# Optimization experiments

Hardware: AMD Instinct MI355X
Metric: run time of the kernel (lower is better)

## Reference

```python
import jax, jax.numpy as jnp
import numpy as np

B, S, H = 2, 1024, 2048
F_DIM = 1408        # per-expert ffn dim
SF_DIM = 5632       # shared expert ffn dim
E = 8               # num_experts
TOP_K = 2
NORM_TOPK_PROB = False


def setup_inputs() -> dict:
    key = jax.random.key(0)
    ks = jax.random.split(key, 9)
    w = lambda k, shp: (jax.random.normal(k, shp, dtype=jnp.float32) * 0.02)
    return {
        "hidden_states": jax.random.normal(ks[0], (B, S, H), dtype=jnp.float32),
        "gate_w": w(ks[1], (E, H)),                 # router Linear(H -> E), no bias
        "gate_proj_w": w(ks[2], (E, F_DIM, H)),     # stacked expert gate_proj weights
        "up_proj_w": w(ks[3], (E, F_DIM, H)),
        "down_proj_w": w(ks[4], (E, H, F_DIM)),
        "shared_gate_proj_w": w(ks[5], (SF_DIM, H)),
        "shared_up_proj_w": w(ks[6], (SF_DIM, H)),
        "shared_down_proj_w": w(ks[7], (H, SF_DIM)),
        "shared_expert_gate_w": w(ks[8], (1, H)),   # Linear(H -> 1), no bias
    }


def reference(hidden_states, gate_w, gate_proj_w, up_proj_w, down_proj_w,
              shared_gate_proj_w, shared_up_proj_w, shared_down_proj_w,
              shared_expert_gate_w):
    b, s, h = hidden_states.shape
    x = hidden_states.reshape(-1, h)                              # [T, H]
    # router: softmax in fp32 -> top_k
    logits = x @ gate_w.T                                         # [T, E]
    probs = jax.nn.softmax(logits.astype(jnp.float32), axis=-1)
    rw, sel = jax.lax.top_k(probs, TOP_K)                         # [T, K]
    if NORM_TOPK_PROB:
        rw = rw / jnp.sum(rw, axis=-1, keepdims=True)
    rw = rw.astype(x.dtype)
    # dense one-hot dispatch weights [T, E]
    wm = jnp.sum(jax.nn.one_hot(sel, E, dtype=rw.dtype) * rw[..., None], axis=1)
    # all experts on all tokens (dense dispatch, as in the original)
    g = jax.nn.silu(jnp.einsum('th,efh->tef', x, gate_proj_w))    # [T, E, F]
    u = jnp.einsum('th,efh->tef', x, up_proj_w)
    routed = jnp.einsum('tef,ehf,te->th', g * u, down_proj_w, wm) # [T, H]
    # shared expert with scalar sigmoid gate
    sg = jax.nn.silu(x @ shared_gate_proj_w.T) * (x @ shared_up_proj_w.T)
    shared = sg @ shared_down_proj_w.T                            # [T, H]
    gate_val = jax.nn.sigmoid(x @ shared_expert_gate_w.T)         # [T, 1]
    out = routed + gate_val * shared
    return out.reshape(b, s, h)
```

## Files before the change

kernel.cpp:

```cpp
#include <hip/hip_runtime.h>

#define TT 2048
#define HD 2048
#define FD 1408
#define SFD 5632
#define NE 8
#define BM 128
#define BN 128
#define BK 32

using f32x4 = __attribute__((ext_vector_type(4))) float;
using s16x8 = __attribute__((ext_vector_type(8))) short;
typedef unsigned short us;

__device__ __forceinline__ us f2bf(float f) {
    union { float f; unsigned u; } v; v.f = f;
    unsigned r = v.u + 0x7fff + ((v.u >> 16) & 1);
    return (us)(r >> 16);
}
__device__ __forceinline__ float bf2f(us u) {
    union { unsigned u; float f; } v; v.u = ((unsigned)u) << 16;
    return v.f;
}
__device__ __forceinline__ unsigned cvt2(float a, float b) {
    union { float f; unsigned u; } va, vb; va.f = a; vb.f = b;
    unsigned ra = va.u + 0x8000u, rb = vb.u + 0x8000u;
    return (rb & 0xffff0000u) | (ra >> 16);
}
__device__ __forceinline__ s16x8 pack8(f32x4 h0, f32x4 h1) {
    union { unsigned u[4]; s16x8 s; } r;
    r.u[0] = cvt2(h0[0], h0[1]); r.u[1] = cvt2(h0[2], h0[3]);
    r.u[2] = cvt2(h1[0], h1[1]); r.u[3] = cvt2(h1[2], h1[3]);
    return r.s;
}

__device__ __forceinline__ void gload16(const void* g, void* l) {
    __builtin_amdgcn_global_load_lds(
        (const __attribute__((address_space(1))) unsigned*)g,
        (__attribute__((address_space(3))) unsigned*)l, 16, 0, 0);
}

__global__ void cvt_kernel(const float* __restrict__ x, us* __restrict__ xb) {
    size_t i = ((size_t)blockIdx.x * 256 + threadIdx.x) * 8;
    float4 f0 = *(const float4*)(x + i);
    float4 f1 = *(const float4*)(x + i + 4);
    s16x8 v;
    v[0]=(short)f2bf(f0.x); v[1]=(short)f2bf(f0.y); v[2]=(short)f2bf(f0.z); v[3]=(short)f2bf(f0.w);
    v[4]=(short)f2bf(f1.x); v[5]=(short)f2bf(f1.y); v[6]=(short)f2bf(f1.z); v[7]=(short)f2bf(f1.w);
    *(s16x8*)(xb + i) = v;
}

__global__ void router_kernel(const float* __restrict__ x, const float* __restrict__ gw,
                              const float* __restrict__ segw,
                              int* counts, int* tlist, float* wlist, float* gateval,
                              int* selpos) {
    int wave = threadIdx.x >> 6;
    int lane = threadIdx.x & 63;
    int t = blockIdx.x * 4 + wave;
    float acc[9];
    #pragma unroll
    for (int i = 0; i < 9; ++i) acc[i] = 0.f;
    const float* xrow = x + (size_t)t * HD;
    for (int h = lane; h < HD; h += 64) {
        float xv = xrow[h];
        #pragma unroll
        for (int e = 0; e < NE; ++e) acc[e] += xv * gw[e * HD + h];
        acc[8] += xv * segw[h];
    }
    #pragma unroll
    for (int i = 0; i < 9; ++i) {
        float v = acc[i];
        #pragma unroll
        for (int s = 32; s > 0; s >>= 1) v += __shfl_xor(v, s);
        acc[i] = v;
    }
    if (lane == 0) {
        float m = acc[0];
        #pragma unroll
        for (int e = 1; e < NE; ++e) m = fmaxf(m, acc[e]);
        float p[NE], sum = 0.f;
        #pragma unroll
        for (int e = 0; e < NE; ++e) { p[e] = expf(acc[e] - m); sum += p[e]; }
        float inv = 1.f / sum;
        int b1 = 0, b2 = -1; float v1 = p[0], v2 = -1.f;
        #pragma unroll
        for (int e = 1; e < NE; ++e) {
            if (p[e] > v1) { v2 = v1; b2 = b1; v1 = p[e]; b1 = e; }
            else if (p[e] > v2) { v2 = p[e]; b2 = e; }
        }
        v1 *= inv; v2 *= inv;
        int s1 = atomicAdd(&counts[b1], 1); tlist[b1 * TT + s1] = t; wlist[b1 * TT + s1] = v1;
        int s2 = atomicAdd(&counts[b2], 1); tlist[b2 * TT + s2] = t; wlist[b2 * TT + s2] = v2;
        selpos[2 * t]     = b1 * TT + s1;
        selpos[2 * t + 1] = b2 * TT + s2;
        gateval[t] = 1.f / (1.f + expf(-acc[8]));
    }
}

__global__ void prefix_kernel(const int* counts, int* offsets) {
    if (threadIdx.x == 0) {
        int s = 0;
        for (int e = 0; e < NE; ++e) { offsets[e] = s; s += counts[e]; }
    }
}

__global__ void combine_full(const int* __restrict__ selpos, const float* __restrict__ wlist,
                             const int* __restrict__ offsets, const float* __restrict__ gateval,
                             const float* __restrict__ sdpart, const us* __restrict__ robuf,
                             float* __restrict__ out) {
    int t = blockIdx.x;
    int p0 = selpos[2 * t], p1 = selpos[2 * t + 1];
    float w0 = wlist[p0], w1 = wlist[p1];
    int r0 = offsets[p0 >> 11] + (p0 & (TT - 1));
    int r1 = offsets[p1 >> 11] + (p1 & (TT - 1));
    float g = gateval[t];
    int c = threadIdx.x * 8;
    const float* s0 = sdpart + (size_t)t * HD + c;
    const float* s1 = sdpart + (size_t)TT * HD + (size_t)t * HD + c;
    s16x8 a = *(const s16x8*)(robuf + (size_t)r0 * HD + c);
    s16x8 b = *(const s16x8*)(robuf + (size_t)r1 * HD + c);
    float* op = out + (size_t)t * HD + c;
    #pragma unroll
    for (int j = 0; j < 8; ++j)
        op[j] = g * (s0[j] + s1[j]) + w0 * bf2f((us)a[j]) + w1 * bf2f((us)b[j]);
}

__global__ void combine_add(const int* __restrict__ selpos, const float* __restrict__ wlist,
                            const int* __restrict__ offsets,
                            const us* __restrict__ robuf, float* __restrict__ out) {
    int t = blockIdx.x;
    int p0 = selpos[2 * t], p1 = selpos[2 * t + 1];
    float w0 = wlist[p0], w1 = wlist[p1];
    int r0 = offsets[p0 >> 11] + (p0 & (TT - 1));
    int r1 = offsets[p1 >> 11] + (p1 & (TT - 1));
    int c = threadIdx.x * 8;
    s16x8 a = *(const s16x8*)(robuf + (size_t)r0 * HD + c);
    s16x8 b = *(const s16x8*)(robuf + (size_t)r1 * HD + c);
    float* op = out + (size_t)t * HD + c;
    #pragma unroll
    for (int j = 0; j < 8; ++j)
        op[j] += w0 * bf2f((us)a[j]) + w1 * bf2f((us)b[j]);
}

#define GU_TOT   2112
#define GU_CHUNK (GU_TOT / 8)
#define DN_TOT   2560
#define DN_CHUNK (DN_TOT / 8)

__global__ __launch_bounds__(256, 3)
void gemm6(const us* __restrict__ xb,
           const us* __restrict__ Bg_s, const us* __restrict__ Bu_s,
           const us* __restrict__ Bg_r, const us* __restrict__ Bu_r,
           us* __restrict__ Cs, us* __restrict__ Cr,
           const int* __restrict__ counts, const int* __restrict__ offsets,
           const int* __restrict__ tlist) {
    __shared__ s16x8 Asl[2][512];
    __shared__ s16x8 B0l[2][512];
    __shared__ s16x8 B1l[2][512];

    int hw = blockIdx.x;
    int flat = (hw & 7) * GU_CHUNK + (hw >> 3);
    int pi = flat >> 4, mt = flat & 15;
    int grpIdx = pi / 3, pos = pi % 3;
    int z, nt;
    if (pos == 0) { z = 0; nt = grpIdx; }
    else { int ri = grpIdx * 2 + (pos - 1);
           z = 1 + ri / 11; nt = ri % 11; }

    bool sp = (z == 0);
    int e = z - 1;
    int M = sp ? TT : counts[e];
    int n0 = nt * BN;
    int m0 = mt * BM;
    if (M == 0 || m0 >= M) return;
    int row_off = sp ? 0 : offsets[e];
    const us* B0p = sp ? Bg_s : Bg_r + (size_t)e * FD * HD;
    const us* B1p = sp ? Bu_s : Bu_r + (size_t)e * FD * HD;

    int tid = threadIdx.x;
    int lane = tid & 63, w = tid >> 6;

    const us* aptr[2];
    const us* b0ptr[2];
    const us* b1ptr[2];
    #pragma unroll
    for (int j = 0; j < 2; ++j) {
        int r = 32 * w + 16 * j + (lane >> 2);
        int c = (lane & 3) ^ ((r >> 1) & 3);
        int ar = m0 + r; if (ar > M - 1) ar = M - 1;
        size_t arow = sp ? (size_t)ar : (size_t)tlist[e * TT + ar];
        aptr[j]  = xb + arow * HD + c * 8;
        b0ptr[j] = B0p + (size_t)(n0 + r) * HD + c * 8;
        b1ptr[j] = B1p + (size_t)(n0 + r) * HD + c * 8;
    }

    int wm = (w >> 1) * 64, wn = (w & 1) * 64;
    int grp = lane >> 4, l16 = lane & 15;

    f32x4 acc0[4][4], acc1[4][4];
    f32x4 zero = {0.f, 0.f, 0.f, 0.f};
    #pragma unroll
    for (int mi = 0; mi < 4; ++mi)
        #pragma unroll
        for (int ni = 0; ni < 4; ++ni) { acc0[mi][ni] = zero; acc1[mi][ni] = zero; }

    auto stage = [&](int buf, int k0) {
        #pragma unroll
        for (int j = 0; j < 2; ++j)
            gload16(aptr[j] + k0, (void*)&Asl[buf][(32 * w + 16 * j) * 4]);
        #pragma unroll
        for (int j = 0; j < 2; ++j)
            gload16(b0ptr[j] + k0, (void*)&B0l[buf][(32 * w + 16 * j) * 4]);
        #pragma unroll
        for (int j = 0; j < 2; ++j)
            gload16(b1ptr[j] + k0, (void*)&B1l[buf][(32 * w + 16 * j) * 4]);
    };

    stage(0, 0);
    int cur = 0;
    const int NT = HD / BK;
    for (int kt = 0; kt < NT; ++kt) {
        __syncthreads();
        if (kt + 1 < NT) stage(cur ^ 1, (kt + 1) * BK);
        s16x8 af[4];
        #pragma unroll
        for (int mi = 0; mi < 4; ++mi) {
            int rr = wm + mi * 16 + l16;
            af[mi] = Asl[cur][rr * 4 + (grp ^ ((rr >> 1) & 3))];
        }
        #pragma unroll
        for (int ni = 0; ni < 4; ++ni) {
            int rb = wn + ni * 16 + l16;
            int slot = rb * 4 + (grp ^ ((rb >> 1) & 3));
            s16x8 b0 = B0l[cur][slot];
            #pragma unroll
            for (int mi = 0; mi < 4; ++mi)
                acc0[mi][ni] = __builtin_amdgcn_mfma_f32_16x16x32_bf16(af[mi], b0, acc0[mi][ni], 0, 0, 0);
            s16x8 b1 = B1l[cur][slot];
            #pragma unroll
            for (int mi = 0; mi < 4; ++mi)
                acc1[mi][ni] = __builtin_amdgcn_mfma_f32_16x16x32_bf16(af[mi], b1, acc1[mi][ni], 0, 0, 0);
        }
        cur ^= 1;
    }

    #pragma unroll
    for (int mi = 0; mi < 4; ++mi) {
        #pragma unroll
        for (int r_ = 0; r_ < 4; ++r_) {
            int mrow = m0 + wm + mi * 16 + (lane >> 4) * 4 + r_;
            if (mrow >= M) continue;
            #pragma unroll
            for (int ni = 0; ni < 4; ++ni) {
                int col = n0 + wn + ni * 16 + l16;
                float g = acc0[mi][ni][r_], u = acc1[mi][ni][r_];
                float val = g * u / (1.f + __expf(-g));
                if (sp) Cs[(size_t)mrow * SFD + col] = f2bf(val);
                else    Cr[(size_t)(row_off + mrow) * FD + col] = f2bf(val);
            }
        }
    }
}

__global__ __launch_bounds__(256, 3)
void gemm_down(const us* __restrict__ Ashared, const us* __restrict__ Arouted,
               const us* __restrict__ Bshared, const us* __restrict__ Brouted,
               float* __restrict__ Cshared, us* __restrict__ Crouted,
               const int* __restrict__ counts, const int* __restrict__ offsets) {
    __shared__ s16x8 Asl[2][512];
    __shared__ s16x8 Bsl[2][512];

    int hw = blockIdx.x;
    int flat = (hw & 7) * DN_CHUNK + (hw >> 3);
    int pi = flat >> 4, mt = flat & 15;
    int grpIdx = pi / 5, pos = pi % 5;
    int z, nt;
    if (pos == 0) { z = grpIdx >> 4; nt = grpIdx & 15; }
    else { int ri = grpIdx * 4 + (pos - 1);
           z = 2 + (ri >> 4); nt = ri & 15; }

    bool sp = (z < 2);
    int e = z - 2;
    int M = sp ? TT : counts[e];
    int n0 = nt * BN;
    int m0 = mt * BM;
    if (M == 0 || m0 >= M) return;
    int row_off = sp ? 0 : offsets[e];
    int NT = sp ? (SFD / 2 / BK) : (FD / BK);
    int lda = sp ? SFD : FD;
    int kofs = sp ? z * (SFD / 2) : 0;
    const us* Abase = (sp ? Ashared : Arouted) + kofs;
    const us* Bbase = (sp ? Bshared : Brouted + (size_t)e * HD * FD) + kofs;

    int tid = threadIdx.x;
    int lane = tid & 63, w = tid >> 6;

    const us* aptr[2];
    const us* bptr[2];
    #pragma unroll
    for (int j = 0; j < 2; ++j) {
        int r = 32 * w + 16 * j + (lane >> 2);
        int c = (lane & 3) ^ ((r >> 1) & 3);
        int ar = m0 + r; if (ar > M - 1) ar = M - 1;
        size_t arow = sp ? (size_t)ar : (size_t)(row_off + ar);
        aptr[j] = Abase + arow * lda + c * 8;
        bptr[j] = Bbase + (size_t)(n0 + r) * lda + c * 8;
    }

    int wm = (w >> 1) * 64, wn = (w & 1) * 64;
    int grp = lane >> 4, l16 = lane & 15;

    f32x4 acc[4][4];
    f32x4 zero = {0.f, 0.f, 0.f, 0.f};
    #pragma unroll
    for (int mi = 0; mi < 4; ++mi)
        #pragma unroll
        for (int ni = 0; ni < 4; ++ni) acc[mi][ni] = zero;

    auto stage = [&](int buf, int k0) {
        #pragma unroll
        for (int j = 0; j < 2; ++j)
            gload16(aptr[j] + k0, (void*)&Asl[buf][(32 * w + 16 * j) * 4]);
        #pragma unroll
        for (int j = 0; j < 2; ++j)
            gload16(bptr[j] + k0, (void*)&Bsl[buf][(32 * w + 16 * j) * 4]);
    };

    stage(0, 0);
    int cur = 0;
    for (int kt = 0; kt < NT; ++kt) {
        __syncthreads();
        if (kt + 1 < NT) stage(cur ^ 1, (kt + 1) * BK);
        s16x8 af[4];
        #pragma unroll
        for (int mi = 0; mi < 4; ++mi) {
            int rr = wm + mi * 16 + l16;
            af[mi] = Asl[cur][rr * 4 + (grp ^ ((rr >> 1) & 3))];
        }
        #pragma unroll
        for (int ni = 0; ni < 4; ++ni) {
            int rb = wn + ni * 16 + l16;
            s16x8 bf = Bsl[cur][rb * 4 + (grp ^ ((rb >> 1) & 3))];
            #pragma unroll
            for (int mi = 0; mi < 4; ++mi)
                acc[mi][ni] = __builtin_amdgcn_mfma_f32_16x16x32_bf16(af[mi], bf, acc[mi][ni], 0, 0, 0);
        }
        cur ^= 1;
    }

    #pragma unroll
    for (int mi = 0; mi < 4; ++mi) {
        #pragma unroll
        for (int r_ = 0; r_ < 4; ++r_) {
            int mrow = m0 + wm + mi * 16 + (lane >> 4) * 4 + r_;
            if (mrow >= M) continue;
            #pragma unroll
            for (int ni = 0; ni < 4; ++ni) {
                int col = n0 + wn + ni * 16 + l16;
                float v = acc[mi][ni][r_];
                if (sp) Cshared[(size_t)z * TT * HD + (size_t)mrow * HD + col] = v;
                else    Crouted[(size_t)(row_off + mrow) * HD + col] = f2bf(v);
            }
        }
    }
}

template<int EPI, bool GATHER>
__global__ __launch_bounds__(256, 2)
void gemm4(const us* __restrict__ A, int lda,
           const float* __restrict__ B, size_t eStrideB, int ldb, int K,
           int Mfixed, const int* __restrict__ counts, const int* __restrict__ offsets,
           const int* __restrict__ tlist, const float* __restrict__ wlist,
           us* __restrict__ C, int ldc,
           const float* __restrict__ gateval, float* __restrict__ out, int ldout) {
    __shared__ s16x8 As[3][512];
    __shared__ f32x4 Bs[3][1024];

    int e = blockIdx.z;
    int M = counts ? counts[e] : Mfixed;
    int n0 = blockIdx.x * BN;
    int m0 = blockIdx.y * BM;
    if (M == 0 || m0 >= M) return;
    int row_off = offsets ? offsets[e] : 0;
    const float* Bp = B + (size_t)e * eStrideB;

    int tid = threadIdx.x;
    int lane = tid & 63, w = tid >> 6;

    const us* aptr[2];
    #pragma unroll
    for (int j = 0; j < 2; ++j) {
        int r = 32 * w + 16 * j + (lane >> 2);
        int c = (lane & 3) ^ (r & 3);
        int ar = m0 + r; if (ar > M - 1) ar = M - 1;
        size_t grow;
        if constexpr (GATHER) grow = (size_t)tlist[e * TT + ar];
        else                  grow = (size_t)(row_off + ar);
        aptr[j] = A + grow * (size_t)lda + c * 8;
    }
    const float* bptr[4];
    #pragma unroll
    for (int j = 0; j < 4; ++j) {
        int r = 32 * w + 8 * j + (lane >> 3);
        int c = (lane & 7) ^ (r & 7);
        bptr[j] = Bp + (size_t)(n0 + r) * ldb + c * 4;
    }

    int wm = (w >> 1) * 64, wn = (w & 1) * 64;
    int grp = lane >> 4, l16 = lane & 15;

    f32x4 acc[4][4];
    f32x4 zero = {0.f, 0.f, 0.f, 0.f};
    #pragma unroll
    for (int mi = 0; mi < 4; ++mi)
        #pragma unroll
        for (int ni = 0; ni < 4; ++ni) acc[mi][ni] = zero;

    auto stage = [&](int buf, int k0) {
        #pragma unroll
        for (int j = 0; j < 2; ++j)
            gload16(aptr[j] + k0, (void*)&As[buf][(32 * w + 16 * j) * 4]);
        #pragma unroll
        for (int j = 0; j < 4; ++j)
            gload16(bptr[j] + k0, (void*)&Bs[buf][(32 * w + 8 * j) * 8]);
    };

    int NT = K / BK;
    stage(0, 0);
    stage(1, BK);
    for (int kt = 0; kt < NT; ++kt) {
        int cur = kt % 3;
        __builtin_amdgcn_s_barrier();
        if (kt + 2 < NT) {
            stage((kt + 2) % 3, (kt + 2) * BK);
            asm volatile("s_waitcnt vmcnt(12)" ::: "memory");
        } else if (kt + 1 < NT) {
            asm volatile("s_waitcnt vmcnt(6)" ::: "memory");
        } else {
            asm volatile("s_waitcnt vmcnt(0)" ::: "memory");
        }
        s16x8 af[4];
        #pragma unroll
        for (int mi = 0; mi < 4; ++mi) {
            int rr = wm + mi * 16 + l16;
            af[mi] = As[cur][rr * 4 + (grp ^ (rr & 3))];
        }
        #pragma unroll
        for (int ni = 0; ni < 4; ++ni) {
            int rb = wn + ni * 16 + l16;
            int s0 = (2 * grp) ^ (rb & 7);
            f32x4 h0 = Bs[cur][rb * 8 + s0];
            f32x4 h1 = Bs[cur][rb * 8 + (s0 ^ 1)];
            s16x8 bfr = pack8(h0, h1);
            #pragma unroll
            for (int mi = 0; mi < 4; ++mi)
                acc[mi][ni] = __builtin_amdgcn_mfma_f32_16x16x32_bf16(af[mi], bfr, acc[mi][ni], 0, 0, 0);
        }
    }

    #pragma unroll
    for (int mi = 0; mi < 4; ++mi) {
        #pragma unroll
        for (int r_ = 0; r_ < 4; ++r_) {
            int mrow = m0 + wm + mi * 16 + (lane >> 4) * 4 + r_;
            if (mrow >= M) continue;
            #pragma unroll
            for (int ni = 0; ni < 4; ++ni) {
                int col = n0 + wn + ni * 16 + l16;
                float v = acc[mi][ni][r_];
                if constexpr (EPI == 0) {
                    C[(size_t)(row_off + mrow) * ldc + col] = f2bf(v);
                } else if constexpr (EPI == 1) {
                    size_t idx = (size_t)(row_off + mrow) * ldc + col;
                    float g = bf2f(C[idx]);
                    C[idx] = f2bf(g * v / (1.f + __expf(-g)));
                } else if constexpr (EPI == 2) {
                    int tok = tlist[e * TT + mrow]; float wv = wlist[e * TT + mrow];
                    atomicAdd(out + (size_t)tok * ldout + col, wv * v);
                } else {
                    out[(size_t)mrow * ldout + col] = gateval[mrow] * v;
                }
            }
        }
    }
}

extern "C" void kernel_launch(void* const* d_in, const int* in_sizes, int n_in,
                              void* d_out, int out_size, void* d_ws, size_t ws_size,
                              hipStream_t stream) {
    const float* x    = (const float*)d_in[0];
    const float* gw   = (const float*)d_in[1];
    const float* gpw  = (const float*)d_in[2];
    const float* upw  = (const float*)d_in[3];
    const float* dpw  = (const float*)d_in[4];
    const float* sgw  = (const float*)d_in[5];
    const float* suw  = (const float*)d_in[6];
    const float* sdw  = (const float*)d_in[7];
    const float* segw = (const float*)d_in[8];
    float* out = (float*)d_out;
    char* ws = (char*)d_ws;

    int*   counts  = (int*)(ws + 0);
    int*   offsets = (int*)(ws + 64);
    int*   tlist   = (int*)(ws + 256);
    float* wlist   = (float*)(ws + 65792);
    float* gateval = (float*)(ws + 131328);
    int*   selpos  = (int*)(ws + 139520);

    hipMemsetAsync(counts, 0, 64, stream);
    router_kernel<<<dim3(TT / 4), 256, 0, stream>>>(x, gw, segw, counts, tlist, wlist, gateval, selpos);
    prefix_kernel<<<dim3(1), 64, 0, stream>>>(counts, offsets);

    size_t need_main = 301203456ull;
    if (ws_size >= need_main) {
        us* xb     = (us*)(ws + 262144);
        us* gpw_b  = (us*)(ws + 8650752);
        us* upw_b  = (us*)(ws + 54788096);
        us* dpw_b  = (us*)(ws + 100925440);
        us* sgw_b  = (us*)(ws + 147062784);
        us* suw_b  = (us*)(ws + 170131456);
        us* sdw_b  = (us*)(ws + 193200128);
        us* gbuf_s = (us*)(ws + 216268800);
        us* gbuf_r = (us*)(ws + 239337472);
        us* robuf  = (us*)(ws + 250871808);
        float* sdpart = (float*)(ws + 267649024);

        cvt_kernel<<<dim3(TT * HD / 2048), 256, 0, stream>>>(x, xb);
        cvt_kernel<<<dim3(NE * FD * HD / 2048), 256, 0, stream>>>(gpw, gpw_b);
        cvt_kernel<<<dim3(NE * FD * HD / 2048), 256, 0, stream>>>(upw, upw_b);
        cvt_kernel<<<dim3(NE * HD * FD / 2048), 256, 0, stream>>>(dpw, dpw_b);
        cvt_kernel<<<dim3(SFD * HD / 2048), 256, 0, stream>>>(sgw, sgw_b);
        cvt_kernel<<<dim3(SFD * HD / 2048), 256, 0, stream>>>(suw, suw_b);
        cvt_kernel<<<dim3(HD * SFD / 2048), 256, 0, stream>>>(sdw, sdw_b);

        gemm6<<<dim3(GU_TOT), 256, 0, stream>>>(
            xb, sgw_b, suw_b, gpw_b, upw_b, gbuf_s, gbuf_r, counts, offsets, tlist);
        gemm_down<<<dim3(DN_TOT), 256, 0, stream>>>(
            gbuf_s, gbuf_r, sdw_b, dpw_b, sdpart, robuf, counts, offsets);

        combine_full<<<dim3(TT), 256, 0, stream>>>(selpos, wlist, offsets, gateval, sdpart, robuf, out);
        return;
    }

    us* xb    = (us*)(ws + 155904);
    us* gbuf  = (us*)(ws + 8544512);
    us* robuf = (us*)(ws + 20078848);
    size_t need_fb = 20078848 + (size_t)4096 * HD * 2;

    cvt_kernel<<<dim3(TT * HD / 2048), 256, 0, stream>>>(x, xb);

    gemm4<0, false><<<dim3(SFD / BN, TT / BM, 1), 256, 0, stream>>>(
        xb, HD, sgw, 0, HD, HD, TT, nullptr, nullptr, nullptr, nullptr, gbuf, SFD, nullptr, nullptr, 0);
    gemm4<1, false><<<dim3(SFD / BN, TT / BM, 1), 256, 0, stream>>>(
        xb, HD, suw, 0, HD, HD, TT, nullptr, nullptr, nullptr, nullptr, gbuf, SFD, nullptr, nullptr, 0);
    gemm4<3, false><<<dim3(HD / BN, TT / BM, 1), 256, 0, stream>>>(
        gbuf, SFD, sdw, 0, SFD, SFD, TT, nullptr, nullptr, nullptr, nullptr, nullptr, 0, gateval, out, HD);

    gemm4<0, true><<<dim3(FD / BN, TT / BM, NE), 256, 0, stream>>>(
        xb, HD, gpw, (size_t)FD * HD, HD, HD, 0, counts, offsets, tlist, nullptr, gbuf, FD, nullptr, nullptr, 0);
    gemm4<1, true><<<dim3(FD / BN, TT / BM, NE), 256, 0, stream>>>(
        xb, HD, upw, (size_t)FD * HD, HD, HD, 0, counts, offsets, tlist, nullptr, gbuf, FD, nullptr, nullptr, 0);

    if (ws_size >= need_fb) {
        gemm4<0, false><<<dim3(HD / BN, TT / BM, NE), 256, 0, stream>>>(
            gbuf, FD, dpw, (size_t)HD * FD, FD, FD, 0, counts, offsets, nullptr, nullptr, robuf, HD, nullptr, nullptr, 0);
        combine_add<<<dim3(TT), 256, 0, stream>>>(selpos, wlist, offsets, robuf, out);
    } else {
        gemm4<2, false><<<dim3(HD / BN, TT / BM, NE), 256, 0, stream>>>(
            gbuf, FD, dpw, (size_t)HD * FD, FD, FD, 0, counts, offsets, tlist, wlist, nullptr, 0, nullptr, out, HD);
    }
}
```

Measured before the change: 520.1 us.

## Load fp32 weights directly in GEMMs and convert to bf16 while reading LDS

```diff
diff --git a/kernel.cpp b/kernel.cpp
--- a/kernel.cpp
+++ b/kernel.cpp
@@ -147,16 +147,16 @@
 #define DN_TOT   2560
 #define DN_CHUNK (DN_TOT / 8)
 
-__global__ __launch_bounds__(256, 3)
+__global__ __launch_bounds__(256, 2)
 void gemm6(const us* __restrict__ xb,
-           const us* __restrict__ Bg_s, const us* __restrict__ Bu_s,
-           const us* __restrict__ Bg_r, const us* __restrict__ Bu_r,
+           const float* __restrict__ Bg_s, const float* __restrict__ Bu_s,
+           const float* __restrict__ Bg_r, const float* __restrict__ Bu_r,
            us* __restrict__ Cs, us* __restrict__ Cr,
            const int* __restrict__ counts, const int* __restrict__ offsets,
            const int* __restrict__ tlist) {
     __shared__ s16x8 Asl[2][512];
-    __shared__ s16x8 B0l[2][512];
-    __shared__ s16x8 B1l[2][512];
+    __shared__ f32x4 B0f[2][1024];
+    __shared__ f32x4 B1f[2][1024];
 
     int hw = blockIdx.x;
     int flat = (hw & 7) * GU_CHUNK + (hw >> 3);
@@ -164,8 +164,7 @@
     int grpIdx = pi / 3, pos = pi % 3;
     int z, nt;
     if (pos == 0) { z = 0; nt = grpIdx; }
-    else { int ri = grpIdx * 2 + (pos - 1);
-           z = 1 + ri / 11; nt = ri % 11; }
+    else { int ri = grpIdx * 2 + (pos - 1); z = 1 + ri / 11; nt = ri % 11; }
 
     bool sp = (z == 0);
     int e = z - 1;
@@ -174,24 +173,29 @@
     int m0 = mt * BM;
     if (M == 0 || m0 >= M) return;
     int row_off = sp ? 0 : offsets[e];
-    const us* B0p = sp ? Bg_s : Bg_r + (size_t)e * FD * HD;
-    const us* B1p = sp ? Bu_s : Bu_r + (size_t)e * FD * HD;
+    const float* B0p = sp ? Bg_s : Bg_r + (size_t)e * FD * HD;
+    const float* B1p = sp ? Bu_s : Bu_r + (size_t)e * FD * HD;
 
     int tid = threadIdx.x;
     int lane = tid & 63, w = tid >> 6;
 
     const us* aptr[2];
-    const us* b0ptr[2];
-    const us* b1ptr[2];
     #pragma unroll
     for (int j = 0; j < 2; ++j) {
         int r = 32 * w + 16 * j + (lane >> 2);
         int c = (lane & 3) ^ ((r >> 1) & 3);
         int ar = m0 + r; if (ar > M - 1) ar = M - 1;
         size_t arow = sp ? (size_t)ar : (size_t)tlist[e * TT + ar];
-        aptr[j]  = xb + arow * HD + c * 8;
-        b0ptr[j] = B0p + (size_t)(n0 + r) * HD + c * 8;
-        b1ptr[j] = B1p + (size_t)(n0 + r) * HD + c * 8;
+        aptr[j] = xb + arow * HD + c * 8;
+    }
+    const float* b0ptr[4];
+    const float* b1ptr[4];
+    #pragma unroll
+    for (int j = 0; j < 4; ++j) {
+        int r = 32 * w + 8 * j + (lane >> 3);
+        int c = (lane & 7) ^ (r & 7);
+        b0ptr[j] = B0p + (size_t)(n0 + r) * HD + c * 4;
+        b1ptr[j] = B1p + (size_t)(n0 + r) * HD + c * 4;
     }
 
     int wm = (w >> 1) * 64, wn = (w & 1) * 64;
@@ -209,11 +213,11 @@
         for (int j = 0; j < 2; ++j)
             gload16(aptr[j] + k0, (void*)&Asl[buf][(32 * w + 16 * j) * 4]);
         #pragma unroll
-        for (int j = 0; j < 2; ++j)
-            gload16(b0ptr[j] + k0, (void*)&B0l[buf][(32 * w + 16 * j) * 4]);
-        #pragma unroll
-        for (int j = 0; j < 2; ++j)
-            gload16(b1ptr[j] + k0, (void*)&B1l[buf][(32 * w + 16 * j) * 4]);
+        for (int j = 0; j < 4; ++j)
+            gload16(b0ptr[j] + k0, (void*)&B0f[buf][(32 * w + 8 * j) * 8]);
+        #pragma unroll
+        for (int j = 0; j < 4; ++j)
+            gload16(b1ptr[j] + k0, (void*)&B1f[buf][(32 * w + 8 * j) * 8]);
     };
 
     stage(0, 0);
@@ -231,12 +235,12 @@
         #pragma unroll
         for (int ni = 0; ni < 4; ++ni) {
             int rb = wn + ni * 16 + l16;
-            int slot = rb * 4 + (grp ^ ((rb >> 1) & 3));
-            s16x8 b0 = B0l[cur][slot];
+            int s0 = (2 * grp) ^ (rb & 7);
+            s16x8 b0 = pack8(B0f[cur][rb * 8 + s0], B0f[cur][rb * 8 + (s0 ^ 1)]);
             #pragma unroll
             for (int mi = 0; mi < 4; ++mi)
                 acc0[mi][ni] = __builtin_amdgcn_mfma_f32_16x16x32_bf16(af[mi], b0, acc0[mi][ni], 0, 0, 0);
-            s16x8 b1 = B1l[cur][slot];
+            s16x8 b1 = pack8(B1f[cur][rb * 8 + s0], B1f[cur][rb * 8 + (s0 ^ 1)]);
             #pragma unroll
             for (int mi = 0; mi < 4; ++mi)
                 acc1[mi][ni] = __builtin_amdgcn_mfma_f32_16x16x32_bf16(af[mi], b1, acc1[mi][ni], 0, 0, 0);
@@ -264,11 +268,11 @@
 
 __global__ __launch_bounds__(256, 3)
 void gemm_down(const us* __restrict__ Ashared, const us* __restrict__ Arouted,
-               const us* __restrict__ Bshared, const us* __restrict__ Brouted,
+               const float* __restrict__ Bshared, const float* __restrict__ Brouted,
                float* __restrict__ Cshared, us* __restrict__ Crouted,
                const int* __restrict__ counts, const int* __restrict__ offsets) {
     __shared__ s16x8 Asl[2][512];
-    __shared__ s16x8 Bsl[2][512];
+    __shared__ f32x4 Bf[2][1024];
 
     int hw = blockIdx.x;
     int flat = (hw & 7) * DN_CHUNK + (hw >> 3);
@@ -276,8 +280,7 @@
     int grpIdx = pi / 5, pos = pi % 5;
     int z, nt;
     if (pos == 0) { z = grpIdx >> 4; nt = grpIdx & 15; }
-    else { int ri = grpIdx * 4 + (pos - 1);
-           z = 2 + (ri >> 4); nt = ri & 15; }
+    else { int ri = grpIdx * 4 + (pos - 1); z = 2 + (ri >> 4); nt = ri & 15; }
 
     bool sp = (z < 2);
     int e = z - 2;
@@ -290,13 +293,12 @@
     int lda = sp ? SFD : FD;
     int kofs = sp ? z * (SFD / 2) : 0;
     const us* Abase = (sp ? Ashared : Arouted) + kofs;
-    const us* Bbase = (sp ? Bshared : Brouted + (size_t)e * HD * FD) + kofs;
+    const float* Bbase = (sp ? Bshared : Brouted + (size_t)e * HD * FD) + kofs;
 
     int tid = threadIdx.x;
     int lane = tid & 63, w = tid >> 6;
 
     const us* aptr[2];
-    const us* bptr[2];
     #pragma unroll
     for (int j = 0; j < 2; ++j) {
         int r = 32 * w + 16 * j + (lane >> 2);
@@ -304,7 +306,13 @@
         int ar = m0 + r; if (ar > M - 1) ar = M - 1;
         size_t arow = sp ? (size_t)ar : (size_t)(row_off + ar);
         aptr[j] = Abase + arow * lda + c * 8;
-        bptr[j] = Bbase + (size_t)(n0 + r) * lda + c * 8;
+    }
+    const float* bptr[4];
+    #pragma unroll
+    for (int j = 0; j < 4; ++j) {
+        int r = 32 * w + 8 * j + (lane >> 3);
+        int c = (lane & 7) ^ (r & 7);
+        bptr[j] = Bbase + (size_t)(n0 + r) * lda + c * 4;
     }
 
     int wm = (w >> 1) * 64, wn = (w & 1) * 64;
@@ -322,8 +330,8 @@
         for (int j = 0; j < 2; ++j)
             gload16(aptr[j] + k0, (void*)&Asl[buf][(32 * w + 16 * j) * 4]);
         #pragma unroll
-        for (int j = 0; j < 2; ++j)
-            gload16(bptr[j] + k0, (void*)&Bsl[buf][(32 * w + 16 * j) * 4]);
+        for (int j = 0; j < 4; ++j)
+            gload16(bptr[j] + k0, (void*)&Bf[buf][(32 * w + 8 * j) * 8]);
     };
 
     stage(0, 0);
@@ -340,7 +348,8 @@
         #pragma unroll
         for (int ni = 0; ni < 4; ++ni) {
             int rb = wn + ni * 16 + l16;
-            s16x8 bf = Bsl[cur][rb * 4 + (grp ^ ((rb >> 1) & 3))];
+            int s0 = (2 * grp) ^ (rb & 7);
+            s16x8 bf = pack8(Bf[cur][rb * 8 + s0], Bf[cur][rb * 8 + (s0 ^ 1)]);
             #pragma unroll
             for (int mi = 0; mi < 4; ++mi)
                 acc[mi][ni] = __builtin_amdgcn_mfma_f32_16x16x32_bf16(af[mi], bf, acc[mi][ni], 0, 0, 0);
@@ -511,32 +520,20 @@
     router_kernel<<<dim3(TT / 4), 256, 0, stream>>>(x, gw, segw, counts, tlist, wlist, gateval, selpos);
     prefix_kernel<<<dim3(1), 64, 0, stream>>>(counts, offsets);
 
-    size_t need_main = 301203456ull;
+    size_t need_main = 101974016ull;
     if (ws_size >= need_main) {
         us* xb     = (us*)(ws + 262144);
-        us* gpw_b  = (us*)(ws + 8650752);
-        us* upw_b  = (us*)(ws + 54788096);
-        us* dpw_b  = (us*)(ws + 100925440);
-        us* sgw_b  = (us*)(ws + 147062784);
-        us* suw_b  = (us*)(ws + 170131456);
-        us* sdw_b  = (us*)(ws + 193200128);
-        us* gbuf_s = (us*)(ws + 216268800);
-        us* gbuf_r = (us*)(ws + 239337472);
-        us* robuf  = (us*)(ws + 250871808);
-        float* sdpart = (float*)(ws + 267649024);
+        us* gbuf_s = (us*)(ws + 17039360);
+        us* gbuf_r = (us*)(ws + 40108032);
+        us* robuf  = (us*)(ws + 51642368);
+        float* sdpart = (float*)(ws + 68419584);
 
         cvt_kernel<<<dim3(TT * HD / 2048), 256, 0, stream>>>(x, xb);
-        cvt_kernel<<<dim3(NE * FD * HD / 2048), 256, 0, stream>>>(gpw, gpw_b);
-        cvt_kernel<<<dim3(NE * FD * HD / 2048), 256, 0, stream>>>(upw, upw_b);
-        cvt_kernel<<<dim3(NE * HD * FD / 2048), 256, 0, stream>>>(dpw, dpw_b);
-        cvt_kernel<<<dim3(SFD * HD / 2048), 256, 0, stream>>>(sgw, sgw_b);
-        cvt_kernel<<<dim3(SFD * HD / 2048), 256, 0, stream>>>(suw, suw_b);
-        cvt_kernel<<<dim3(HD * SFD / 2048), 256, 0, stream>>>(sdw, sdw_b);
 
         gemm6<<<dim3(GU_TOT), 256, 0, stream>>>(
-            xb, sgw_b, suw_b, gpw_b, upw_b, gbuf_s, gbuf_r, counts, offsets, tlist);
+            xb, sgw, suw, gpw, upw, gbuf_s, gbuf_r, counts, offsets, tlist);
         gemm_down<<<dim3(DN_TOT), 256, 0, stream>>>(
-            gbuf_s, gbuf_r, sdw_b, dpw_b, sdpart, robuf, counts, offsets);
+            gbuf_s, gbuf_r, sdw, dpw, sdpart, robuf, counts, offsets);
 
         combine_full<<<dim3(TT), 256, 0, stream>>>(selpos, wlist, offsets, gateval, sdpart, robuf, out);
         return;
```

Measured after the change: 733.2 us. 1.41x slower.
